# Kernel optimization log

Hardware: AMD Instinct MI355X
Metric: run time of the kernel (lower is better)

Reference implementation:

```python
import jax, jax.numpy as jnp
import numpy as np

NC, NP, T, E, H = 3000, 30000, 8, 64000, 128

def seg_mean(msgs, idx, n):
    # mean aggregation over destination segments (PyG SAGEConv default aggr='mean')
    s = jax.ops.segment_sum(msgs, idx, num_segments=n)
    c = jax.ops.segment_sum(jnp.ones((idx.shape[0], 1), msgs.dtype), idx, num_segments=n)
    return s / jnp.maximum(c, 1.0)

def gru_last(seq, w_ih, w_hh, b_ih, b_hh):
    # torch.nn.GRU, single layer, seq-first input [T, N, Hin]; returns h at last step
    Hh = w_hh.shape[1]
    def step(h, x):
        gi = x @ w_ih.T + b_ih
        gh = h @ w_hh.T + b_hh
        ir, iz, inn = jnp.split(gi, 3, axis=-1)
        hr, hz, hn = jnp.split(gh, 3, axis=-1)
        r = jax.nn.sigmoid(ir + hr)
        z = jax.nn.sigmoid(iz + hz)
        n = jnp.tanh(inn + r * hn)
        h2 = (1.0 - z) * n + z * h
        return h2, None
    h0 = jnp.zeros((seq.shape[1], Hh), seq.dtype)
    hT, _ = jax.lax.scan(step, h0, seq)
    return hT


def setup_inputs() -> dict:
    key = jax.random.key(0)
    ks = iter(jax.random.split(key, 40))
    f = lambda shp, scale: jax.random.normal(next(ks), shp, jnp.float32) * scale
    inp = {
        'x_country': f((T, NC, 32), 1.0),
        'x_product': f((T, NP, 64), 1.0),
        'edge_src': jax.random.randint(next(ks), (T, E), 0, NC, jnp.int32),
        'edge_dst': jax.random.randint(next(ks), (T, E), 0, NP, jnp.int32),
        'w_clin': f((H, 32), 32 ** -0.5), 'b_clin': f((H,), 0.02),
        'w_plin': f((H, 64), 64 ** -0.5), 'b_plin': f((H,), 0.02),
    }
    for nm in ['wl1_cp', 'wr1_cp', 'wl1_pc', 'wr1_pc', 'wl2_cp', 'wr2_cp', 'wl2_pc', 'wr2_pc']:
        inp[nm] = f((H, H), H ** -0.5)
    for nm in ['bl1_cp', 'bl1_pc', 'bl2_cp', 'bl2_pc']:
        inp[nm] = f((H,), 0.02)
    for nm in ['w_ih_c', 'w_hh_c', 'w_ih_p', 'w_hh_p']:
        inp[nm] = f((3 * H, H), H ** -0.5)
    for nm in ['b_ih_c', 'b_hh_c', 'b_ih_p', 'b_hh_p']:
        inp[nm] = f((3 * H,), 0.02)
    return inp


def reference(x_country, x_product, edge_src, edge_dst,
              w_clin, b_clin, w_plin, b_plin,
              wl1_cp, bl1_cp, wr1_cp, wl1_pc, bl1_pc, wr1_pc,
              wl2_cp, bl2_cp, wr2_cp, wl2_pc, bl2_pc, wr2_pc,
              w_ih_c, w_hh_c, b_ih_c, b_hh_c,
              w_ih_p, w_hh_p, b_ih_p, b_hh_p):

    def encode(xc, xp, es, ed):
        # input projections
        hc = xc @ w_clin.T + b_clin          # [NC, H]
        hp = xp @ w_plin.T + b_plin          # [NP, H]
        # hetero SAGE layer 1 (mean aggr), relu; dropout is identity in eval
        mp = seg_mean(hc[es], ed, NP)        # country -> product messages
        mc = seg_mean(hp[ed], es, NC)        # product -> country messages
        hp1 = jax.nn.relu(mp @ wl1_cp.T + bl1_cp + hp @ wr1_cp.T)
        hc1 = jax.nn.relu(mc @ wl1_pc.T + bl1_pc + hc @ wr1_pc.T)
        # hetero SAGE layer 2, no activation
        mp2 = seg_mean(hc1[es], ed, NP)
        mc2 = seg_mean(hp1[ed], es, NC)
        hp2 = mp2 @ wl2_cp.T + bl2_cp + hp1 @ wr2_cp.T
        hc2 = mc2 @ wl2_pc.T + bl2_pc + hc1 @ wr2_pc.T
        return hc2, hp2

    zc_seq, zp_seq = jax.vmap(encode)(x_country, x_product, edge_src, edge_dst)  # [T,NC,H], [T,NP,H]
    zc = gru_last(zc_seq, w_ih_c, w_hh_c, b_ih_c, b_hh_c)   # [NC, H]
    zp = gru_last(zp_seq, w_ih_p, w_hh_p, b_ih_p, b_hh_p)   # [NP, H]
    return zc, zp
```

## Files before the change

### kernel.cpp

```cpp
#include <hip/hip_runtime.h>

#define NCN 3000
#define NPN 30000
#define TT 8
#define EE 64000
#define HH 128
#define CAPP 24
#define CAPC 64

typedef __attribute__((ext_vector_type(8))) short bf16x8;
typedef __attribute__((ext_vector_type(4))) float f32x4;

__device__ inline unsigned short f2bf(float f) {
    unsigned u = __float_as_uint(f);
    u += 0x7FFF + ((u >> 16) & 1);
    return (unsigned short)(u >> 16);
}
__device__ inline float bf2f(unsigned short h) {
    return __uint_as_float(((unsigned)h) << 16);
}
__device__ inline void split8(const float4 a, const float4 b, bf16x8& hi, bf16x8& lo) {
    float v[8] = {a.x, a.y, a.z, a.w, b.x, b.y, b.z, b.w};
#pragma unroll
    for (int i = 0; i < 8; ++i) {
        unsigned short hs = f2bf(v[i]);
        float rem = v[i] - bf2f(hs);
        hi[i] = (short)hs;
        lo[i] = (short)f2bf(rem);
    }
}
__device__ inline void add4(float4& a, const float4 b) {
    a.x += b.x; a.y += b.y; a.z += b.z; a.w += b.w;
}

__global__ void lin_wprep(const float* __restrict__ w, unsigned short* __restrict__ blob,
                          int K) {
    int idx = blockIdx.x * blockDim.x + threadIdx.x;
    if (idx >= HH * K) return;
    int n = idx / K, k = idx - n * K;
    int nt = n >> 4, nl = n & 15;
    int kc = k >> 5, kg = (k >> 3) & 3, kj = k & 7;
    int KC = K >> 5;
    int base = (nt * KC + kc) * 1024 + (kg * 16 + nl) * 8 + kj;
    float f = w[idx];
    unsigned short hi = f2bf(f), lo = f2bf(f - bf2f(hi));
    blob[base] = hi;
    blob[base + 512] = lo;
}

__global__ void sage_wprep(const float* __restrict__ wl, const float* __restrict__ wr,
                           unsigned short* __restrict__ blob) {
    int idx = blockIdx.x * blockDim.x + threadIdx.x;
    if (idx >= HH * HH) return;
    int n = idx >> 7, k = idx & 127;
    int jt = n >> 4, nl = n & 15;
    int kc = k >> 5, kg = (k >> 3) & 3, kj = k & 7;
    int base = (jt * 4 + kc) * 2048 + (kg * 16 + nl) * 8 + kj;
    float f = wl[idx];
    unsigned short hi = f2bf(f), lo = f2bf(f - bf2f(hi));
    blob[base] = hi;
    blob[base + 512] = lo;
    f = wr[idx];
    hi = f2bf(f); lo = f2bf(f - bf2f(hi));
    blob[base + 1024] = hi;
    blob[base + 1536] = lo;
}

__global__ void gru_wprep(const float* __restrict__ wih, const float* __restrict__ whh,
                          unsigned short* __restrict__ blob) {
    int idx = blockIdx.x * blockDim.x + threadIdx.x;
    if (idx >= 3 * HH * HH) return;
    int n = idx >> 7, k = idx & 127;
    int gate = n >> 7, j128 = n & 127;
    int jt = j128 >> 4, nl = j128 & 15;
    int kc = k >> 5, kg = (k >> 3) & 3, kj = k & 7;
    int base = (jt * 4 + kc) * 6144 + gate * 2048 + (kg * 16 + nl) * 8 + kj;
    float f = wih[idx];
    unsigned short hi = f2bf(f), lo = f2bf(f - bf2f(hi));
    blob[base] = hi;
    blob[base + 512] = lo;
    f = whh[idx];
    hi = f2bf(f); lo = f2bf(f - bf2f(hi));
    blob[base + 1024] = hi;
    blob[base + 1536] = lo;
}

template<int K>
__global__ __launch_bounds__(256, 4)
void linproj_mfma(const float* __restrict__ x, const unsigned short* __restrict__ blob,
                  const float* __restrict__ b, float* __restrict__ out, int N) {
    const int SLOTS = K / 8;
    const int KC = K / 32;
    __shared__ unsigned short lds[2 * 32 * K];
    int i0 = blockIdx.x * 32;
    int tid = threadIdx.x;
    if (tid * 8 < 32 * K) {
        int linear = tid * 8;
        int r = linear / K, k0 = linear % K;
        int row = i0 + r; if (row >= N) row = N - 1;
        float4 a = *(const float4*)&x[(size_t)row * K + k0];
        float4 b4 = *(const float4*)&x[(size_t)row * K + k0 + 4];
        bf16x8 hi, lo;
        split8(a, b4, hi, lo);
        int dst8 = (r * SLOTS + ((k0 >> 3) ^ (r & (SLOTS - 1)))) * 8;
        *(bf16x8*)&lds[dst8] = hi;
        *(bf16x8*)&lds[32 * K + dst8] = lo;
    }
    __syncthreads();
    int wid = tid >> 6, lane = tid & 63;
    int jt0 = wid * 2;
    f32x4 acc[2][2];
#pragma unroll
    for (int a = 0; a < 2; ++a)
#pragma unroll
        for (int m = 0; m < 2; ++m) acc[a][m] = (f32x4){0.f, 0.f, 0.f, 0.f};
#pragma unroll
    for (int kc = 0; kc < KC; ++kc) {
        bf16x8 ah[2], al[2];
#pragma unroll
        for (int mt = 0; mt < 2; ++mt) {
            int rl = mt * 16 + (lane & 15);
            int slot = (kc * 4 + (lane >> 4)) ^ (rl & (SLOTS - 1));
            int aoff = (rl * SLOTS + slot) * 8;
            ah[mt] = *(const bf16x8*)&lds[aoff];
            al[mt] = *(const bf16x8*)&lds[32 * K + aoff];
        }
#pragma unroll
        for (int jj = 0; jj < 2; ++jj) {
            int bbase = ((jt0 + jj) * KC + kc) * 1024 + lane * 8;
            bf16x8 f0 = *(const bf16x8*)&blob[bbase];
            bf16x8 f1 = *(const bf16x8*)&blob[bbase + 512];
#pragma unroll
            for (int mt = 0; mt < 2; ++mt) {
                acc[jj][mt] = __builtin_amdgcn_mfma_f32_16x16x32_bf16(ah[mt], f0, acc[jj][mt], 0, 0, 0);
                acc[jj][mt] = __builtin_amdgcn_mfma_f32_16x16x32_bf16(al[mt], f0, acc[jj][mt], 0, 0, 0);
                acc[jj][mt] = __builtin_amdgcn_mfma_f32_16x16x32_bf16(ah[mt], f1, acc[jj][mt], 0, 0, 0);
            }
        }
    }
#pragma unroll
    for (int jj = 0; jj < 2; ++jj) {
        int j = (jt0 + jj) * 16 + (lane & 15);
        float bv = b[j];
#pragma unroll
        for (int mt = 0; mt < 2; ++mt) {
#pragma unroll
            for (int q = 0; q < 4; ++q) {
                int r_loc = mt * 16 + (lane >> 4) * 4 + q;
                int row = i0 + r_loc;
                if (row < N) out[(size_t)row * HH + j] = acc[jj][mt][q] + bv;
            }
        }
    }
}

__global__ void build_kernel(const int* __restrict__ es, const int* __restrict__ ed,
                             int* __restrict__ cntP, int* __restrict__ cntC,
                             int* __restrict__ listP, int* __restrict__ listC) {
    int g = blockIdx.x * 256 + threadIdx.x;
    if (g >= TT * EE) return;
    int t = g / EE;
    int s = es[g], d = ed[g];
    int pP = atomicAdd(&cntP[t * NPN + d], 1);
    if (pP < CAPP) listP[((size_t)t * NPN + d) * CAPP + pP] = s;
    int pC = atomicAdd(&cntC[t * NCN + s], 1);
    if (pC < CAPC) listC[((size_t)t * NCN + s) * CAPC + pC] = d;
}

__device__ inline void stage512(unsigned short* lds, const int* cnt, const int* list,
                                int CAP, const float* gsrc, const float* hin,
                                int i0, int N, int tid) {
    int r = tid >> 4, k0 = (tid & 15) * 8;
    int row = i0 + r; if (row >= N) row = N - 1;
    float4 ha = *(const float4*)&hin[(size_t)row * HH + k0];
    float4 hb = *(const float4*)&hin[(size_t)row * HH + k0 + 4];
    int ntru = cnt[row];
    int n = ntru > CAP ? CAP : ntru;
    const int* lst = &list[(size_t)row * CAP];
    float4 a0 = {0,0,0,0}, b0 = {0,0,0,0}, a1 = {0,0,0,0}, b1 = {0,0,0,0};
    float4 a2 = {0,0,0,0}, b2 = {0,0,0,0}, a3 = {0,0,0,0}, b3 = {0,0,0,0};
    int e = 0;
    for (; e + 4 <= n; e += 4) {
        int4 ss = *(const int4*)&lst[e];
        const float4* p0 = (const float4*)&gsrc[(size_t)ss.x * HH + k0];
        const float4* p1 = (const float4*)&gsrc[(size_t)ss.y * HH + k0];
        const float4* p2 = (const float4*)&gsrc[(size_t)ss.z * HH + k0];
        const float4* p3 = (const float4*)&gsrc[(size_t)ss.w * HH + k0];
        float4 u0 = p0[0], v0 = p0[1];
        float4 u1 = p1[0], v1 = p1[1];
        float4 u2 = p2[0], v2 = p2[1];
        float4 u3 = p3[0], v3 = p3[1];
        add4(a0, u0); add4(b0, v0);
        add4(a1, u1); add4(b1, v1);
        add4(a2, u2); add4(b2, v2);
        add4(a3, u3); add4(b3, v3);
    }
    for (; e < n; ++e) {
        int s = lst[e];
        const float4* p0 = (const float4*)&gsrc[(size_t)s * HH + k0];
        float4 u0 = p0[0], v0 = p0[1];
        add4(a0, u0); add4(b0, v0);
    }
    add4(a0, a1); add4(b0, b1);
    add4(a2, a3); add4(b2, b3);
    add4(a0, a2); add4(b0, b2);
    float inv = 1.0f / fmaxf((float)ntru, 1.0f);
    a0.x *= inv; a0.y *= inv; a0.z *= inv; a0.w *= inv;
    b0.x *= inv; b0.y *= inv; b0.z *= inv; b0.w *= inv;
    int dst8 = (r * 16 + ((k0 >> 3) ^ (r & 7))) * 8;
    bf16x8 hi, lo;
    split8(a0, b0, hi, lo);
    *(bf16x8*)&lds[dst8] = hi;
    *(bf16x8*)&lds[4096 + dst8] = lo;
    split8(ha, hb, hi, lo);
    *(bf16x8*)&lds[8192 + dst8] = hi;
    *(bf16x8*)&lds[12288 + dst8] = lo;
}

__global__ __launch_bounds__(512, 2)
void pair_kernel(int bndGC, int bndSC, int bndGP,
                 const int* __restrict__ cntP_all, const int* __restrict__ cntC_all,
                 const int* __restrict__ listP_all, const int* __restrict__ listC_all,
                 const float* __restrict__ hp_all, const float* __restrict__ hc_all,
                 float* __restrict__ hp1A, float* __restrict__ hc1A,
                 float* __restrict__ hp1B, float* __restrict__ hc1B,
                 int t_gru, int t_sage,
                 const unsigned short* __restrict__ blob_s1cp, const float* __restrict__ bl1_cp,
                 const unsigned short* __restrict__ blob_s1pc, const float* __restrict__ bl1_pc,
                 const unsigned short* __restrict__ blob_s2cp, const float* __restrict__ bl2_cp,
                 const unsigned short* __restrict__ blob_s2pc, const float* __restrict__ bl2_pc,
                 const unsigned short* __restrict__ blob_gp,
                 const float* __restrict__ b_ih_p, const float* __restrict__ b_hh_p,
                 const unsigned short* __restrict__ blob_gc,
                 const float* __restrict__ b_ih_c, const float* __restrict__ b_hh_c,
                 float* __restrict__ h_c, float* __restrict__ h_p) {
    __shared__ unsigned short lds[4 * 4096];
    int bid = blockIdx.x;
    bool isGru, isC;
    int idx;
    if (bid < bndGC)      { isGru = true;  isC = true;  idx = bid; }
    else if (bid < bndSC) { isGru = false; isC = true;  idx = bid - bndGC; }
    else if (bid < bndGP) { isGru = true;  isC = false; idx = bid - bndSC; }
    else                  { isGru = false; isC = false; idx = bid - bndGP; }

    float* hp1_g = (t_gru & 1) ? hp1B : hp1A;
    float* hc1_g = (t_gru & 1) ? hc1B : hc1A;
    float* hp1_s = (t_sage & 1) ? hp1B : hp1A;
    float* hc1_s = (t_sage & 1) ? hc1B : hc1A;

    const int* cnt; const int* list; int CAP;
    const float* gsrc; const float* hin;
    const unsigned short* sblob; const float* sbl;
    const unsigned short* gblob; const float* bih; const float* bhh;
    float* outp;
    int N, i0 = idx * 32;
    if (isGru) {
        if (isC) {
            cnt = cntC_all + (size_t)t_gru * NCN;
            list = listC_all + (size_t)t_gru * NCN * CAPC; CAP = CAPC;
            gsrc = hp1_g; hin = hc1_g;
            sblob = blob_s2pc; sbl = bl2_pc;
            gblob = blob_gc; bih = b_ih_c; bhh = b_hh_c;
            outp = h_c; N = NCN;
        } else {
            cnt = cntP_all + (size_t)t_gru * NPN;
            list = listP_all + (size_t)t_gru * NPN * CAPP; CAP = CAPP;
            gsrc = hc1_g; hin = hp1_g;
            sblob = blob_s2cp; sbl = bl2_cp;
            gblob = blob_gp; bih = b_ih_p; bhh = b_hh_p;
            outp = h_p; N = NPN;
        }
    } else {
        const float* hp_t = hp_all + (size_t)t_sage * NPN * HH;
        const float* hc_t = hc_all + (size_t)t_sage * NCN * HH;
        if (isC) {
            cnt = cntC_all + (size_t)t_sage * NCN;
            list = listC_all + (size_t)t_sage * NCN * CAPC; CAP = CAPC;
            gsrc = hp_t; hin = hc_t;
            sblob = blob_s1pc; sbl = bl1_pc;
            gblob = nullptr; bih = nullptr; bhh = nullptr;
            outp = hc1_s; N = NCN;
        } else {
            cnt = cntP_all + (size_t)t_sage * NPN;
            list = listP_all + (size_t)t_sage * NPN * CAPP; CAP = CAPP;
            gsrc = hc_t; hin = hp_t;
            sblob = blob_s1cp; sbl = bl1_cp;
            gblob = nullptr; bih = nullptr; bhh = nullptr;
            outp = hp1_s; N = NPN;
        }
    }
    int tid = threadIdx.x;
    stage512(lds, cnt, list, CAP, gsrc, hin, i0, N, tid);
    __syncthreads();
    int wid = tid >> 6, lane = tid & 63;
    int jt = wid;
    f32x4 acc[2];
    acc[0] = (f32x4){0.f, 0.f, 0.f, 0.f};
    acc[1] = (f32x4){0.f, 0.f, 0.f, 0.f};
#pragma unroll
    for (int kc = 0; kc < 4; ++kc) {
        int bbase = (jt * 4 + kc) * 2048 + lane * 8;
        bf16x8 f0 = *(const bf16x8*)&sblob[bbase];
        bf16x8 f1 = *(const bf16x8*)&sblob[bbase + 512];
        bf16x8 f2 = *(const bf16x8*)&sblob[bbase + 1024];
        bf16x8 f3 = *(const bf16x8*)&sblob[bbase + 1536];
#pragma unroll
        for (int mt = 0; mt < 2; ++mt) {
            int rl = mt * 16 + (lane & 15);
            int aoff = (rl * 16 + ((kc * 4 + (lane >> 4)) ^ (rl & 7))) * 8;
            bf16x8 amh = *(const bf16x8*)&lds[aoff];
            bf16x8 aml = *(const bf16x8*)&lds[4096 + aoff];
            bf16x8 ahh = *(const bf16x8*)&lds[8192 + aoff];
            bf16x8 ahl = *(const bf16x8*)&lds[12288 + aoff];
            acc[mt] = __builtin_amdgcn_mfma_f32_16x16x32_bf16(amh, f0, acc[mt], 0, 0, 0);
            acc[mt] = __builtin_amdgcn_mfma_f32_16x16x32_bf16(aml, f0, acc[mt], 0, 0, 0);
            acc[mt] = __builtin_amdgcn_mfma_f32_16x16x32_bf16(amh, f1, acc[mt], 0, 0, 0);
            acc[mt] = __builtin_amdgcn_mfma_f32_16x16x32_bf16(ahh, f2, acc[mt], 0, 0, 0);
            acc[mt] = __builtin_amdgcn_mfma_f32_16x16x32_bf16(ahl, f2, acc[mt], 0, 0, 0);
            acc[mt] = __builtin_amdgcn_mfma_f32_16x16x32_bf16(ahh, f3, acc[mt], 0, 0, 0);
        }
    }
    int j = jt * 16 + (lane & 15);

    if (!isGru) {
        float bv = sbl[j];
#pragma unroll
        for (int mt = 0; mt < 2; ++mt) {
#pragma unroll
            for (int q = 0; q < 4; ++q) {
                int r_loc = mt * 16 + (lane >> 4) * 4 + q;
                int row = i0 + r_loc;
                if (row >= N) continue;
                float v = fmaxf(acc[mt][q] + bv, 0.0f);
                outp[(size_t)row * HH + j] = v;
            }
        }
        return;
    }

    __syncthreads();
    int sr = tid >> 4, sk0 = (tid & 15) * 8;
    {
        int row = i0 + sr; if (row >= N) row = N - 1;
        float4 hl0 = *(const float4*)&outp[(size_t)row * HH + sk0];
        float4 hl1 = *(const float4*)&outp[(size_t)row * HH + sk0 + 4];
        float bv = sbl[j];
#pragma unroll
        for (int mt = 0; mt < 2; ++mt) {
#pragma unroll
            for (int q = 0; q < 4; ++q) {
                int r_loc = mt * 16 + (lane >> 4) * 4 + q;
                float v = acc[mt][q] + bv;
                unsigned short hi = f2bf(v);
                unsigned short lo = f2bf(v - bf2f(hi));
                int off = (r_loc * 16 + ((j >> 3) ^ (r_loc & 7))) * 8 + (j & 7);
                lds[off] = hi;
                lds[4096 + off] = lo;
            }
        }
        int dst8 = (sr * 16 + ((sk0 >> 3) ^ (sr & 7))) * 8;
        bf16x8 hi, lo;
        split8(hl0, hl1, hi, lo);
        *(bf16x8*)&lds[8192 + dst8] = hi;
        *(bf16x8*)&lds[12288 + dst8] = lo;
    }
    __syncthreads();
    f32x4 ar[2], az[2], an[2], ahn[2];
#pragma unroll
    for (int m = 0; m < 2; ++m) {
        ar[m] = (f32x4){0.f, 0.f, 0.f, 0.f};
        az[m] = (f32x4){0.f, 0.f, 0.f, 0.f};
        an[m] = (f32x4){0.f, 0.f, 0.f, 0.f};
        ahn[m] = (f32x4){0.f, 0.f, 0.f, 0.f};
    }
#pragma unroll
    for (int kc = 0; kc < 4; ++kc) {
        bf16x8 axh[2], axl[2], ahh[2], ahl[2];
#pragma unroll
        for (int mt = 0; mt < 2; ++mt) {
            int rl = mt * 16 + (lane & 15);
            int aoff = (rl * 16 + ((kc * 4 + (lane >> 4)) ^ (rl & 7))) * 8;
            axh[mt] = *(const bf16x8*)&lds[aoff];
            axl[mt] = *(const bf16x8*)&lds[4096 + aoff];
            ahh[mt] = *(const bf16x8*)&lds[8192 + aoff];
            ahl[mt] = *(const bf16x8*)&lds[12288 + aoff];
        }
        int bbase = (jt * 4 + kc) * 6144 + lane * 8;
        {
            bf16x8 f0 = *(const bf16x8*)&gblob[bbase];
            bf16x8 f1 = *(const bf16x8*)&gblob[bbase + 512];
            bf16x8 f2 = *(const bf16x8*)&gblob[bbase + 1024];
            bf16x8 f3 = *(const bf16x8*)&gblob[bbase + 1536];
#pragma unroll
            for (int mt = 0; mt < 2; ++mt) {
                ar[mt] = __builtin_amdgcn_mfma_f32_16x16x32_bf16(axh[mt], f0, ar[mt], 0, 0, 0);
                ar[mt] = __builtin_amdgcn_mfma_f32_16x16x32_bf16(axl[mt], f0, ar[mt], 0, 0, 0);
                ar[mt] = __builtin_amdgcn_mfma_f32_16x16x32_bf16(axh[mt], f1, ar[mt], 0, 0, 0);
                ar[mt] = __builtin_amdgcn_mfma_f32_16x16x32_bf16(ahh[mt], f2, ar[mt], 0, 0, 0);
                ar[mt] = __builtin_amdgcn_mfma_f32_16x16x32_bf16(ahl[mt], f2, ar[mt], 0, 0, 0);
                ar[mt] = __builtin_amdgcn_mfma_f32_16x16x32_bf16(ahh[mt], f3, ar[mt], 0, 0, 0);
            }
        }
        {
            bf16x8 f0 = *(const bf16x8*)&gblob[bbase + 2048];
            bf16x8 f1 = *(const bf16x8*)&gblob[bbase + 2560];
            bf16x8 f2 = *(const bf16x8*)&gblob[bbase + 3072];
            bf16x8 f3 = *(const bf16x8*)&gblob[bbase + 3584];
#pragma unroll
            for (int mt = 0; mt < 2; ++mt) {
                az[mt] = __builtin_amdgcn_mfma_f32_16x16x32_bf16(axh[mt], f0, az[mt], 0, 0, 0);
                az[mt] = __builtin_amdgcn_mfma_f32_16x16x32_bf16(axl[mt], f0, az[mt], 0, 0, 0);
                az[mt] = __builtin_amdgcn_mfma_f32_16x16x32_bf16(axh[mt], f1, az[mt], 0, 0, 0);
                az[mt] = __builtin_amdgcn_mfma_f32_16x16x32_bf16(ahh[mt], f2, az[mt], 0, 0, 0);
                az[mt] = __builtin_amdgcn_mfma_f32_16x16x32_bf16(ahl[mt], f2, az[mt], 0, 0, 0);
                az[mt] = __builtin_amdgcn_mfma_f32_16x16x32_bf16(ahh[mt], f3, az[mt], 0, 0, 0);
            }
        }
        {
            bf16x8 f0 = *(const bf16x8*)&gblob[bbase + 4096];
            bf16x8 f1 = *(const bf16x8*)&gblob[bbase + 4608];
            bf16x8 f2 = *(const bf16x8*)&gblob[bbase + 5120];
            bf16x8 f3 = *(const bf16x8*)&gblob[bbase + 5632];
#pragma unroll
            for (int mt = 0; mt < 2; ++mt) {
                an[mt] = __builtin_amdgcn_mfma_f32_16x16x32_bf16(axh[mt], f0, an[mt], 0, 0, 0);
                an[mt] = __builtin_amdgcn_mfma_f32_16x16x32_bf16(axl[mt], f0, an[mt], 0, 0, 0);
                an[mt] = __builtin_amdgcn_mfma_f32_16x16x32_bf16(axh[mt], f1, an[mt], 0, 0, 0);
                ahn[mt] = __builtin_amdgcn_mfma_f32_16x16x32_bf16(ahh[mt], f2, ahn[mt], 0, 0, 0);
                ahn[mt] = __builtin_amdgcn_mfma_f32_16x16x32_bf16(ahl[mt], f2, ahn[mt], 0, 0, 0);
                ahn[mt] = __builtin_amdgcn_mfma_f32_16x16x32_bf16(ahh[mt], f3, ahn[mt], 0, 0, 0);
            }
        }
    }
    {
        float br = bih[j] + bhh[j];
        float bz = bih[HH + j] + bhh[HH + j];
        float bn_i = bih[2 * HH + j];
        float bn_h = bhh[2 * HH + j];
#pragma unroll
        for (int mt = 0; mt < 2; ++mt) {
#pragma unroll
            for (int q = 0; q < 4; ++q) {
                int r_loc = mt * 16 + (lane >> 4) * 4 + q;
                int row = i0 + r_loc;
                if (row >= N) continue;
                float pr = ar[mt][q] + br;
                float pz = az[mt][q] + bz;
                float pn = an[mt][q] + bn_i;
                float phn = ahn[mt][q] + bn_h;
                float rg = 1.0f / (1.0f + __expf(-pr));
                float zg = 1.0f / (1.0f + __expf(-pz));
                float ng = tanhf(pn + rg * phn);
                int eo = (r_loc * 16 + ((j >> 3) ^ (r_loc & 7))) * 8 + (j & 7);
                float hprev = bf2f(lds[8192 + eo]) + bf2f(lds[12288 + eo]);
                outp[(size_t)row * HH + j] = (1.0f - zg) * ng + zg * hprev;
            }
        }
    }
}

extern "C" void kernel_launch(void* const* d_in, const int* in_sizes, int n_in,
                              void* d_out, int out_size, void* d_ws, size_t ws_size,
                              hipStream_t stream) {
    const float* xc     = (const float*)d_in[0];
    const float* xp     = (const float*)d_in[1];
    const int*   esrc   = (const int*)d_in[2];
    const int*   edst   = (const int*)d_in[3];
    const float* w_clin = (const float*)d_in[4];
    const float* b_clin = (const float*)d_in[5];
    const float* w_plin = (const float*)d_in[6];
    const float* b_plin = (const float*)d_in[7];
    const float* wl1_cp = (const float*)d_in[8];
    const float* wr1_cp = (const float*)d_in[9];
    const float* wl1_pc = (const float*)d_in[10];
    const float* wr1_pc = (const float*)d_in[11];
    const float* wl2_cp = (const float*)d_in[12];
    const float* wr2_cp = (const float*)d_in[13];
    const float* wl2_pc = (const float*)d_in[14];
    const float* wr2_pc = (const float*)d_in[15];
    const float* bl1_cp = (const float*)d_in[16];
    const float* bl1_pc = (const float*)d_in[17];
    const float* bl2_cp = (const float*)d_in[18];
    const float* bl2_pc = (const float*)d_in[19];
    const float* w_ih_c = (const float*)d_in[20];
    const float* w_hh_c = (const float*)d_in[21];
    const float* w_ih_p = (const float*)d_in[22];
    const float* w_hh_p = (const float*)d_in[23];
    const float* b_ih_c = (const float*)d_in[24];
    const float* b_hh_c = (const float*)d_in[25];
    const float* b_ih_p = (const float*)d_in[26];
    const float* b_hh_p = (const float*)d_in[27];

    float* ws      = (float*)d_ws;
    float* hp_all  = ws;
    float* hc_all  = hp_all + (size_t)TT * NPN * HH;
    float* hp1A    = hc_all + (size_t)TT * NCN * HH;
    float* hc1A    = hp1A + (size_t)NPN * HH;
    float* hp1B    = hc1A + (size_t)NCN * HH;
    float* hc1B    = hp1B + (size_t)NPN * HH;
    int*   cntP_all = (int*)(hc1B + (size_t)NCN * HH);
    int*   cntC_all = cntP_all + (size_t)TT * NPN;
    int*   listP_all = cntC_all + (size_t)TT * NCN;
    int*   listC_all = listP_all + (size_t)TT * NPN * CAPP;

    unsigned short* fw = (unsigned short*)(listC_all + (size_t)TT * NCN * CAPC);
    const int SB = 65536;
    const int GB = 196608;
    unsigned short* blob_s1cp = fw;
    unsigned short* blob_s1pc = blob_s1cp + SB;
    unsigned short* blob_s2cp = blob_s1pc + SB;
    unsigned short* blob_s2pc = blob_s2cp + SB;
    unsigned short* blob_gp   = blob_s2pc + SB;
    unsigned short* blob_gc   = blob_gp + GB;
    unsigned short* blob_lc   = blob_gc + GB;
    unsigned short* blob_lp   = blob_lc + 8192;

    float* h_c = (float*)d_out;
    float* h_p = h_c + (size_t)NCN * HH;

    {
        const int B = 256;
        int gs = (HH * HH + B - 1) / B;
        sage_wprep<<<gs, B, 0, stream>>>(wl1_cp, wr1_cp, blob_s1cp);
        sage_wprep<<<gs, B, 0, stream>>>(wl1_pc, wr1_pc, blob_s1pc);
        sage_wprep<<<gs, B, 0, stream>>>(wl2_cp, wr2_cp, blob_s2cp);
        sage_wprep<<<gs, B, 0, stream>>>(wl2_pc, wr2_pc, blob_s2pc);
        int gg = (3 * HH * HH + B - 1) / B;
        gru_wprep<<<gg, B, 0, stream>>>(w_ih_p, w_hh_p, blob_gp);
        gru_wprep<<<gg, B, 0, stream>>>(w_ih_c, w_hh_c, blob_gc);
        lin_wprep<<<(HH * 32 + B - 1) / B, B, 0, stream>>>(w_clin, blob_lc, 32);
        lin_wprep<<<(HH * 64 + B - 1) / B, B, 0, stream>>>(w_plin, blob_lp, 64);
    }

    hipMemsetAsync(d_out, 0, (size_t)out_size * sizeof(float), stream);
    hipMemsetAsync(cntP_all, 0, (size_t)TT * (NPN + NCN) * sizeof(int), stream);

    build_kernel<<<(TT * EE + 255) / 256, 256, 0, stream>>>(esrc, edst, cntP_all, cntC_all,
                                                            listP_all, listC_all);
    linproj_mfma<32><<<(TT * NCN + 31) / 32, 256, 0, stream>>>(xc, blob_lc, b_clin, hc_all, TT * NCN);
    linproj_mfma<64><<<(TT * NPN + 31) / 32, 256, 0, stream>>>(xp, blob_lp, b_plin, hp_all, TT * NPN);

    const int gP32 = (NPN + 31) / 32, gC32 = (NCN + 31) / 32;

    for (int k = 0; k <= TT; ++k) {
        int hasG = (k >= 1), hasS = (k < TT);
        int t_g = hasG ? (k - 1) : 0;
        int t_s = hasS ? k : 0;
        int bndGC = hasG ? gC32 : 0;
        int bndSC = bndGC + (hasS ? gC32 : 0);
        int bndGP = bndSC + (hasG ? gP32 : 0);
        int grid  = bndGP + (hasS ? gP32 : 0);
        pair_kernel<<<grid, 512, 0, stream>>>(
            bndGC, bndSC, bndGP,
            cntP_all, cntC_all, listP_all, listC_all,
            hp_all, hc_all, hp1A, hc1A, hp1B, hc1B,
            t_g, t_s,
            blob_s1cp, bl1_cp, blob_s1pc, bl1_pc,
            blob_s2cp, bl2_cp, blob_s2pc, bl2_pc,
            blob_gp, b_ih_p, b_hh_p,
            blob_gc, b_ih_c, b_hh_c,
            h_c, h_p);
    }
}
```

Before: 651.1 us.

## Double pair_kernel row tile to 64 and reuse GRU weight fragments across tiles

Each block of pair_kernel now handles 64 rows instead of 32, so LDS grows to 64 KB and every wave runs four MFMA row tiles. SAGE and GRU weight fragments loaded from global memory are therefore reused across twice as many rows, and the GRU loop loads all twelve fragments once per k-chunk rather than per gate. The GRU previous hidden state is prefetched before staging so its latency overlaps the gather. The costs are a halved grid, higher register pressure from 4×4 accumulators, and more LDS per block, which may lower occupancy under launch_bounds(512,2).

```diff
diff --git a/kernel.cpp b/kernel.cpp
--- a/kernel.cpp
+++ b/kernel.cpp
@@ -167,54 +167,58 @@
     if (pC < CAPC) listC[((size_t)t * NCN + s) * CAPC + pC] = d;
 }
 
-__device__ inline void stage512(unsigned short* lds, const int* cnt, const int* list,
-                                int CAP, const float* gsrc, const float* hin,
-                                int i0, int N, int tid) {
-    int r = tid >> 4, k0 = (tid & 15) * 8;
-    int row = i0 + r; if (row >= N) row = N - 1;
-    float4 ha = *(const float4*)&hin[(size_t)row * HH + k0];
-    float4 hb = *(const float4*)&hin[(size_t)row * HH + k0 + 4];
-    int ntru = cnt[row];
-    int n = ntru > CAP ? CAP : ntru;
-    const int* lst = &list[(size_t)row * CAP];
-    float4 a0 = {0,0,0,0}, b0 = {0,0,0,0}, a1 = {0,0,0,0}, b1 = {0,0,0,0};
-    float4 a2 = {0,0,0,0}, b2 = {0,0,0,0}, a3 = {0,0,0,0}, b3 = {0,0,0,0};
-    int e = 0;
-    for (; e + 4 <= n; e += 4) {
-        int4 ss = *(const int4*)&lst[e];
-        const float4* p0 = (const float4*)&gsrc[(size_t)ss.x * HH + k0];
-        const float4* p1 = (const float4*)&gsrc[(size_t)ss.y * HH + k0];
-        const float4* p2 = (const float4*)&gsrc[(size_t)ss.z * HH + k0];
-        const float4* p3 = (const float4*)&gsrc[(size_t)ss.w * HH + k0];
-        float4 u0 = p0[0], v0 = p0[1];
-        float4 u1 = p1[0], v1 = p1[1];
-        float4 u2 = p2[0], v2 = p2[1];
-        float4 u3 = p3[0], v3 = p3[1];
-        add4(a0, u0); add4(b0, v0);
-        add4(a1, u1); add4(b1, v1);
-        add4(a2, u2); add4(b2, v2);
-        add4(a3, u3); add4(b3, v3);
-    }
-    for (; e < n; ++e) {
-        int s = lst[e];
-        const float4* p0 = (const float4*)&gsrc[(size_t)s * HH + k0];
-        float4 u0 = p0[0], v0 = p0[1];
-        add4(a0, u0); add4(b0, v0);
-    }
-    add4(a0, a1); add4(b0, b1);
-    add4(a2, a3); add4(b2, b3);
-    add4(a0, a2); add4(b0, b2);
-    float inv = 1.0f / fmaxf((float)ntru, 1.0f);
-    a0.x *= inv; a0.y *= inv; a0.z *= inv; a0.w *= inv;
-    b0.x *= inv; b0.y *= inv; b0.z *= inv; b0.w *= inv;
-    int dst8 = (r * 16 + ((k0 >> 3) ^ (r & 7))) * 8;
-    bf16x8 hi, lo;
-    split8(a0, b0, hi, lo);
-    *(bf16x8*)&lds[dst8] = hi;
-    *(bf16x8*)&lds[4096 + dst8] = lo;
-    split8(ha, hb, hi, lo);
-    *(bf16x8*)&lds[8192 + dst8] = hi;
-    *(bf16x8*)&lds[12288 + dst8] = lo;
+__device__ inline void stage64(unsigned short* lds, const int* cnt, const int* list,
+                               int CAP, const float* gsrc, const float* hin,
+                               int i0, int N, int tid) {
+    int r0 = tid >> 4, k0 = (tid & 15) * 8;
+#pragma unroll
+    for (int h = 0; h < 2; ++h) {
+        int r = r0 + h * 32;
+        int row = i0 + r; if (row >= N) row = N - 1;
+        float4 ha = *(const float4*)&hin[(size_t)row * HH + k0];
+        float4 hb = *(const float4*)&hin[(size_t)row * HH + k0 + 4];
+        int ntru = cnt[row];
+        int n = ntru > CAP ? CAP : ntru;
+        const int* lst = &list[(size_t)row * CAP];
+        float4 a0 = {0,0,0,0}, b0 = {0,0,0,0}, a1 = {0,0,0,0}, b1 = {0,0,0,0};
+        float4 a2 = {0,0,0,0}, b2 = {0,0,0,0}, a3 = {0,0,0,0}, b3 = {0,0,0,0};
+        int e = 0;
+        for (; e + 4 <= n; e += 4) {
+            int4 ss = *(const int4*)&lst[e];
+            const float4* p0 = (const float4*)&gsrc[(size_t)ss.x * HH + k0];
+            const float4* p1 = (const float4*)&gsrc[(size_t)ss.y * HH + k0];
+            const float4* p2 = (const float4*)&gsrc[(size_t)ss.z * HH + k0];
+            const float4* p3 = (const float4*)&gsrc[(size_t)ss.w * HH + k0];
+            float4 u0 = p0[0], v0 = p0[1];
+            float4 u1 = p1[0], v1 = p1[1];
+            float4 u2 = p2[0], v2 = p2[1];
+            float4 u3 = p3[0], v3 = p3[1];
+            add4(a0, u0); add4(b0, v0);
+            add4(a1, u1); add4(b1, v1);
+            add4(a2, u2); add4(b2, v2);
+            add4(a3, u3); add4(b3, v3);
+        }
+        for (; e < n; ++e) {
+            int s = lst[e];
+            const float4* p0 = (const float4*)&gsrc[(size_t)s * HH + k0];
+            float4 u0 = p0[0], v0 = p0[1];
+            add4(a0, u0); add4(b0, v0);
+        }
+        add4(a0, a1); add4(b0, b1);
+        add4(a2, a3); add4(b2, b3);
+        add4(a0, a2); add4(b0, b2);
+        float inv = 1.0f / fmaxf((float)ntru, 1.0f);
+        a0.x *= inv; a0.y *= inv; a0.z *= inv; a0.w *= inv;
+        b0.x *= inv; b0.y *= inv; b0.z *= inv; b0.w *= inv;
+        int dst8 = (r * 16 + ((k0 >> 3) ^ (r & 7))) * 8;
+        bf16x8 hi, lo;
+        split8(a0, b0, hi, lo);
+        *(bf16x8*)&lds[dst8] = hi;
+        *(bf16x8*)&lds[8192 + dst8] = lo;
+        split8(ha, hb, hi, lo);
+        *(bf16x8*)&lds[16384 + dst8] = hi;
+        *(bf16x8*)&lds[24576 + dst8] = lo;
+    }
 }
 
 __global__ __launch_bounds__(512, 2)
@@ -234,7 +238,7 @@
                  const unsigned short* __restrict__ blob_gc,
                  const float* __restrict__ b_ih_c, const float* __restrict__ b_hh_c,
                  float* __restrict__ h_c, float* __restrict__ h_p) {
-    __shared__ unsigned short lds[4 * 4096];
+    __shared__ unsigned short lds[4 * 8192];
     int bid = blockIdx.x;
     bool isGru, isC;
     int idx;
@@ -253,7 +257,7 @@
     const unsigned short* sblob; const float* sbl;
     const unsigned short* gblob; const float* bih; const float* bhh;
     float* outp;
-    int N, i0 = idx * 32;
+    int N, i0 = idx * 64;
     if (isGru) {
         if (isC) {
             cnt = cntC_all + (size_t)t_gru * NCN;
@@ -290,13 +294,26 @@
         }
     }
     int tid = threadIdx.x;
-    stage512(lds, cnt, list, CAP, gsrc, hin, i0, N, tid);
-    __syncthreads();
     int wid = tid >> 6, lane = tid & 63;
     int jt = wid;
-    f32x4 acc[2];
-    acc[0] = (f32x4){0.f, 0.f, 0.f, 0.f};
-    acc[1] = (f32x4){0.f, 0.f, 0.f, 0.f};
+    int sr = tid >> 4, sk0 = (tid & 15) * 8;
+
+    float4 hpre[2][2];
+    if (isGru) {
+#pragma unroll
+        for (int h = 0; h < 2; ++h) {
+            int row = i0 + sr + h * 32; if (row >= N) row = N - 1;
+            hpre[h][0] = *(const float4*)&outp[(size_t)row * HH + sk0];
+            hpre[h][1] = *(const float4*)&outp[(size_t)row * HH + sk0 + 4];
+        }
+    }
+
+    stage64(lds, cnt, list, CAP, gsrc, hin, i0, N, tid);
+    __syncthreads();
+
+    f32x4 acc[4];
+#pragma unroll
+    for (int m = 0; m < 4; ++m) acc[m] = (f32x4){0.f, 0.f, 0.f, 0.f};
 #pragma unroll
     for (int kc = 0; kc < 4; ++kc) {
         int bbase = (jt * 4 + kc) * 2048 + lane * 8;
@@ -305,13 +322,13 @@
         bf16x8 f2 = *(const bf16x8*)&sblob[bbase + 1024];
         bf16x8 f3 = *(const bf16x8*)&sblob[bbase + 1536];
 #pragma unroll
-        for (int mt = 0; mt < 2; ++mt) {
+        for (int mt = 0; mt < 4; ++mt) {
             int rl = mt * 16 + (lane & 15);
             int aoff = (rl * 16 + ((kc * 4 + (lane >> 4)) ^ (rl & 7))) * 8;
             bf16x8 amh = *(const bf16x8*)&lds[aoff];
-            bf16x8 aml = *(const bf16x8*)&lds[4096 + aoff];
-            bf16x8 ahh = *(const bf16x8*)&lds[8192 + aoff];
-            bf16x8 ahl = *(const bf16x8*)&lds[12288 + aoff];
+            bf16x8 aml = *(const bf16x8*)&lds[8192 + aoff];
+            bf16x8 ahh = *(const bf16x8*)&lds[16384 + aoff];
+            bf16x8 ahl = *(const bf16x8*)&lds[24576 + aoff];
             acc[mt] = __builtin_amdgcn_mfma_f32_16x16x32_bf16(amh, f0, acc[mt], 0, 0, 0);
             acc[mt] = __builtin_amdgcn_mfma_f32_16x16x32_bf16(aml, f0, acc[mt], 0, 0, 0);
             acc[mt] = __builtin_amdgcn_mfma_f32_16x16x32_bf16(amh, f1, acc[mt], 0, 0, 0);
@@ -325,7 +342,7 @@
     if (!isGru) {
         float bv = sbl[j];
 #pragma unroll
-        for (int mt = 0; mt < 2; ++mt) {
+        for (int mt = 0; mt < 4; ++mt) {
 #pragma unroll
             for (int q = 0; q < 4; ++q) {
                 int r_loc = mt * 16 + (lane >> 4) * 4 + q;
@@ -339,14 +356,10 @@
     }
 
     __syncthreads();
-    int sr = tid >> 4, sk0 = (tid & 15) * 8;
     {
-        int row = i0 + sr; if (row >= N) row = N - 1;
-        float4 hl0 = *(const float4*)&outp[(size_t)row * HH + sk0];
-        float4 hl1 = *(const float4*)&outp[(size_t)row * HH + sk0 + 4];
         float bv = sbl[j];
 #pragma unroll
-        for (int mt = 0; mt < 2; ++mt) {
+        for (int mt = 0; mt < 4; ++mt) {
 #pragma unroll
             for (int q = 0; q < 4; ++q) {
                 int r_loc = mt * 16 + (lane >> 4) * 4 + q;
@@ -355,19 +368,24 @@
                 unsigned short lo = f2bf(v - bf2f(hi));
                 int off = (r_loc * 16 + ((j >> 3) ^ (r_loc & 7))) * 8 + (j & 7);
                 lds[off] = hi;
-                lds[4096 + off] = lo;
+                lds[8192 + off] = lo;
             }
         }
-        int dst8 = (sr * 16 + ((sk0 >> 3) ^ (sr & 7))) * 8;
-        bf16x8 hi, lo;
-        split8(hl0, hl1, hi, lo);
-        *(bf16x8*)&lds[8192 + dst8] = hi;
-        *(bf16x8*)&lds[12288 + dst8] = lo;
+#pragma unroll
+        for (int h = 0; h < 2; ++h) {
+            int r = sr + h * 32;
+            int dst8 = (r * 16 + ((sk0 >> 3) ^ (r & 7))) * 8;
+            bf16x8 hi, lo;
+            split8(hpre[h][0], hpre[h][1], hi, lo);
+            *(bf16x8*)&lds[16384 + dst8] = hi;
+            *(bf16x8*)&lds[24576 + dst8] = lo;
+        }
     }
     __syncthreads();
-    f32x4 ar[2], az[2], an[2], ahn[2];
-#pragma unroll
-    for (int m = 0; m < 2; ++m) {
+
+    f32x4 ar[4], az[4], an[4], ahn[4];
+#pragma unroll
+    for (int m = 0; m < 4; ++m) {
         ar[m] = (f32x4){0.f, 0.f, 0.f, 0.f};
         az[m] = (f32x4){0.f, 0.f, 0.f, 0.f};
         an[m] = (f32x4){0.f, 0.f, 0.f, 0.f};
@@ -375,61 +393,45 @@
     }
 #pragma unroll
     for (int kc = 0; kc < 4; ++kc) {
-        bf16x8 axh[2], axl[2], ahh[2], ahl[2];
-#pragma unroll
-        for (int mt = 0; mt < 2; ++mt) {
+        int bbase = (jt * 4 + kc) * 6144 + lane * 8;
+        bf16x8 r0 = *(const bf16x8*)&gblob[bbase];
+        bf16x8 r1 = *(const bf16x8*)&gblob[bbase + 512];
+        bf16x8 r2 = *(const bf16x8*)&gblob[bbase + 1024];
+        bf16x8 r3 = *(const bf16x8*)&gblob[bbase + 1536];
+        bf16x8 z0 = *(const bf16x8*)&gblob[bbase + 2048];
+        bf16x8 z1 = *(const bf16x8*)&gblob[bbase + 2560];
+        bf16x8 z2 = *(const bf16x8*)&gblob[bbase + 3072];
+        bf16x8 z3 = *(const bf16x8*)&gblob[bbase + 3584];
+        bf16x8 n0 = *(const bf16x8*)&gblob[bbase + 4096];
+        bf16x8 n1 = *(const bf16x8*)&gblob[bbase + 4608];
+        bf16x8 n2 = *(const bf16x8*)&gblob[bbase + 5120];
+        bf16x8 n3 = *(const bf16x8*)&gblob[bbase + 5632];
+#pragma unroll
+        for (int mt = 0; mt < 4; ++mt) {
             int rl = mt * 16 + (lane & 15);
             int aoff = (rl * 16 + ((kc * 4 + (lane >> 4)) ^ (rl & 7))) * 8;
-            axh[mt] = *(const bf16x8*)&lds[aoff];
-            axl[mt] = *(const bf16x8*)&lds[4096 + aoff];
-            ahh[mt] = *(const bf16x8*)&lds[8192 + aoff];
-            ahl[mt] = *(const bf16x8*)&lds[12288 + aoff];
-        }
-        int bbase = (jt * 4 + kc) * 6144 + lane * 8;
-        {
-            bf16x8 f0 = *(const bf16x8*)&gblob[bbase];
-            bf16x8 f1 = *(const bf16x8*)&gblob[bbase + 512];
-            bf16x8 f2 = *(const bf16x8*)&gblob[bbase + 1024];
-            bf16x8 f3 = *(const bf16x8*)&gblob[bbase + 1536];
-#pragma unroll
-            for (int mt = 0; mt < 2; ++mt) {
-                ar[mt] = __builtin_amdgcn_mfma_f32_16x16x32_bf16(axh[mt], f0, ar[mt], 0, 0, 0);
-                ar[mt] = __builtin_amdgcn_mfma_f32_16x16x32_bf16(axl[mt], f0, ar[mt], 0, 0, 0);
-                ar[mt] = __builtin_amdgcn_mfma_f32_16x16x32_bf16(axh[mt], f1, ar[mt], 0, 0, 0);
-                ar[mt] = __builtin_amdgcn_mfma_f32_16x16x32_bf16(ahh[mt], f2, ar[mt], 0, 0, 0);
-                ar[mt] = __builtin_amdgcn_mfma_f32_16x16x32_bf16(ahl[mt], f2, ar[mt], 0, 0, 0);
-                ar[mt] = __builtin_amdgcn_mfma_f32_16x16x32_bf16(ahh[mt], f3, ar[mt], 0, 0, 0);
-            }
-        }
-        {
-            bf16x8 f0 = *(const bf16x8*)&gblob[bbase + 2048];
-            bf16x8 f1 = *(const bf16x8*)&gblob[bbase + 2560];
-            bf16x8 f2 = *(const bf16x8*)&gblob[bbase + 3072];
-            bf16x8 f3 = *(const bf16x8*)&gblob[bbase + 3584];
-#pragma unroll
-            for (int mt = 0; mt < 2; ++mt) {
-                az[mt] = __builtin_amdgcn_mfma_f32_16x16x32_bf16(axh[mt], f0, az[mt], 0, 0, 0);
-                az[mt] = __builtin_amdgcn_mfma_f32_16x16x32_bf16(axl[mt], f0, az[mt], 0, 0, 0);
-                az[mt] = __builtin_amdgcn_mfma_f32_16x16x32_bf16(axh[mt], f1, az[mt], 0, 0, 0);
-                az[mt] = __builtin_amdgcn_mfma_f32_16x16x32_bf16(ahh[mt], f2, az[mt], 0, 0, 0);
-                az[mt] = __builtin_amdgcn_mfma_f32_16x16x32_bf16(ahl[mt], f2, az[mt], 0, 0, 0);
-                az[mt] = __builtin_amdgcn_mfma_f32_16x16x32_bf16(ahh[mt], f3, az[mt], 0, 0, 0);
-            }
-        }
-        {
-            bf16x8 f0 = *(const bf16x8*)&gblob[bbase + 4096];
-            bf16x8 f1 = *(const bf16x8*)&gblob[bbase + 4608];
-            bf16x8 f2 = *(const bf16x8*)&gblob[bbase + 5120];
-            bf16x8 f3 = *(const bf16x8*)&gblob[bbase + 5632];
-#pragma unroll
-            for (int mt = 0; mt < 2; ++mt) {
-                an[mt] = __builtin_amdgcn_mfma_f32_16x16x32_bf16(axh[mt], f0, an[mt], 0, 0, 0);
-                an[mt] = __builtin_amdgcn_mfma_f32_16x16x32_bf16(axl[mt], f0, an[mt], 0, 0, 0);
-                an[mt] = __builtin_amdgcn_mfma_f32_16x16x32_bf16(axh[mt], f1, an[mt], 0, 0, 0);
-                ahn[mt] = __builtin_amdgcn_mfma_f32_16x16x32_bf16(ahh[mt], f2, ahn[mt], 0, 0, 0);
-                ahn[mt] = __builtin_amdgcn_mfma_f32_16x16x32_bf16(ahl[mt], f2, ahn[mt], 0, 0, 0);
-                ahn[mt] = __builtin_amdgcn_mfma_f32_16x16x32_bf16(ahh[mt], f3, ahn[mt], 0, 0, 0);
-            }
+            bf16x8 axh = *(const bf16x8*)&lds[aoff];
+            bf16x8 axl = *(const bf16x8*)&lds[8192 + aoff];
+            bf16x8 ahh = *(const bf16x8*)&lds[16384 + aoff];
+            bf16x8 ahl = *(const bf16x8*)&lds[24576 + aoff];
+            ar[mt] = __builtin_amdgcn_mfma_f32_16x16x32_bf16(axh, r0, ar[mt], 0, 0, 0);
+            ar[mt] = __builtin_amdgcn_mfma_f32_16x16x32_bf16(axl, r0, ar[mt], 0, 0, 0);
+            ar[mt] = __builtin_amdgcn_mfma_f32_16x16x32_bf16(axh, r1, ar[mt], 0, 0, 0);
+            ar[mt] = __builtin_amdgcn_mfma_f32_16x16x32_bf16(ahh, r2, ar[mt], 0, 0, 0);
+            ar[mt] = __builtin_amdgcn_mfma_f32_16x16x32_bf16(ahl, r2, ar[mt], 0, 0, 0);
+            ar[mt] = __builtin_amdgcn_mfma_f32_16x16x32_bf16(ahh, r3, ar[mt], 0, 0, 0);
+            az[mt] = __builtin_amdgcn_mfma_f32_16x16x32_bf16(axh, z0, az[mt], 0, 0, 0);
+            az[mt] = __builtin_amdgcn_mfma_f32_16x16x32_bf16(axl, z0, az[mt], 0, 0, 0);
+            az[mt] = __builtin_amdgcn_mfma_f32_16x16x32_bf16(axh, z1, az[mt], 0, 0, 0);
+            az[mt] = __builtin_amdgcn_mfma_f32_16x16x32_bf16(ahh, z2, az[mt], 0, 0, 0);
+            az[mt] = __builtin_amdgcn_mfma_f32_16x16x32_bf16(ahl, z2, az[mt], 0, 0, 0);
+            az[mt] = __builtin_amdgcn_mfma_f32_16x16x32_bf16(ahh, z3, az[mt], 0, 0, 0);
+            an[mt] = __builtin_amdgcn_mfma_f32_16x16x32_bf16(axh, n0, an[mt], 0, 0, 0);
+            an[mt] = __builtin_amdgcn_mfma_f32_16x16x32_bf16(axl, n0, an[mt], 0, 0, 0);
+            an[mt] = __builtin_amdgcn_mfma_f32_16x16x32_bf16(axh, n1, an[mt], 0, 0, 0);
+            ahn[mt] = __builtin_amdgcn_mfma_f32_16x16x32_bf16(ahh, n2, ahn[mt], 0, 0, 0);
+            ahn[mt] = __builtin_amdgcn_mfma_f32_16x16x32_bf16(ahl, n2, ahn[mt], 0, 0, 0);
+            ahn[mt] = __builtin_amdgcn_mfma_f32_16x16x32_bf16(ahh, n3, ahn[mt], 0, 0, 0);
         }
     }
     {
@@ -438,7 +440,7 @@
         float bn_i = bih[2 * HH + j];
         float bn_h = bhh[2 * HH + j];
 #pragma unroll
-        for (int mt = 0; mt < 2; ++mt) {
+        for (int mt = 0; mt < 4; ++mt) {
 #pragma unroll
             for (int q = 0; q < 4; ++q) {
                 int r_loc = mt * 16 + (lane >> 4) * 4 + q;
@@ -452,7 +454,7 @@
                 float zg = 1.0f / (1.0f + __expf(-pz));
                 float ng = tanhf(pn + rg * phn);
                 int eo = (r_loc * 16 + ((j >> 3) ^ (r_loc & 7))) * 8 + (j & 7);
-                float hprev = bf2f(lds[8192 + eo]) + bf2f(lds[12288 + eo]);
+                float hprev = bf2f(lds[16384 + eo]) + bf2f(lds[24576 + eo]);
                 outp[(size_t)row * HH + j] = (1.0f - zg) * ng + zg * hprev;
             }
         }
@@ -540,16 +542,16 @@
     linproj_mfma<32><<<(TT * NCN + 31) / 32, 256, 0, stream>>>(xc, blob_lc, b_clin, hc_all, TT * NCN);
     linproj_mfma<64><<<(TT * NPN + 31) / 32, 256, 0, stream>>>(xp, blob_lp, b_plin, hp_all, TT * NPN);
 
-    const int gP32 = (NPN + 31) / 32, gC32 = (NCN + 31) / 32;
+    const int gP64 = (NPN + 63) / 64, gC64 = (NCN + 63) / 64;
 
     for (int k = 0; k <= TT; ++k) {
         int hasG = (k >= 1), hasS = (k < TT);
         int t_g = hasG ? (k - 1) : 0;
         int t_s = hasS ? k : 0;
-        int bndGC = hasG ? gC32 : 0;
-        int bndSC = bndGC + (hasS ? gC32 : 0);
-        int bndGP = bndSC + (hasG ? gP32 : 0);
-        int grid  = bndGP + (hasS ? gP32 : 0);
+        int bndGC = hasG ? gC64 : 0;
+        int bndSC = bndGC + (hasS ? gC64 : 0);
+        int bndGP = bndSC + (hasG ? gP64 : 0);
+        int grid  = bndGP + (hasS ? gP64 : 0);
         pair_kernel<<<grid, 512, 0, stream>>>(
             bndGC, bndSC, bndGP,
             cntP_all, cntC_all, listP_all, listC_all,
```

Measured after the change: 788.4 us. 21.1% more time.
